# Kernel optimization log

Hardware: AMD Instinct MI355X
Metric: run time of the kernel (lower is better)

The kernel has to match this reference:

```python
import jax, jax.numpy as jnp
import numpy as np

HID = 768
POS = 768
TGT = 20
LBL = 30522
EPS = 1e-5


def layer_norm(x, g, b):
    mu = jnp.mean(x, axis=-1, keepdims=True)
    var = jnp.mean((x - mu) ** 2, axis=-1, keepdims=True)
    return (x - mu) * jax.lax.rsqrt(var + EPS) * g + b


def setup_inputs() -> dict:
    key = jax.random.key(0)
    ks = jax.random.split(key, 12)
    bs, n_node, num_pairs = 4, 512, 128
    inp = {
        "input_nodes": jax.random.normal(ks[0], (bs, n_node, HID), dtype=jnp.float32),
        "pairs": jax.random.randint(ks[1], (bs, num_pairs, 2), 0, n_node - 1, dtype=jnp.int64),
        "pos_emb": jax.random.normal(ks[2], (TGT, POS), dtype=jnp.float32) * 0.02,
        "W1": jax.random.normal(ks[3], (2 * HID + POS, HID), dtype=jnp.float32) * 0.02,
        "b1": jnp.zeros((HID,), dtype=jnp.float32),
        "g1": jnp.ones((HID,), dtype=jnp.float32),
        "be1": jnp.zeros((HID,), dtype=jnp.float32),
        "W2": jax.random.normal(ks[4], (HID, HID), dtype=jnp.float32) * 0.02,
        "b2": jnp.zeros((HID,), dtype=jnp.float32),
        "g2": jnp.ones((HID,), dtype=jnp.float32),
        "be2": jnp.zeros((HID,), dtype=jnp.float32),
        "Wd": jax.random.normal(ks[5], (HID, LBL), dtype=jnp.float32) * 0.02,
        "bd": jnp.zeros((LBL,), dtype=jnp.float32),
    }
    return inp


def reference(input_nodes, pairs, pos_emb, W1, b1, g1, be1, W2, b2, g2, be2, Wd, bd):
    bs, num_pairs, _ = pairs.shape
    dim = input_nodes.shape[-1]
    left = pairs[:, :, 0] + 1   # [bs, np]
    right = pairs[:, :, 1] + 1
    # gather paired node features: [bs, np, dim]
    lh = jnp.take_along_axis(input_nodes, left[:, :, None], axis=1)
    rh = jnp.take_along_axis(input_nodes, right[:, :, None], axis=1)
    R = bs * num_pairs
    lh = jnp.broadcast_to(lh.reshape(R, 1, dim), (R, TGT, dim))
    rh = jnp.broadcast_to(rh.reshape(R, 1, dim), (R, TGT, dim))
    pe = jnp.broadcast_to(pos_emb[None, :, :], (R, TGT, POS))
    x = jnp.concatenate((lh, rh, pe), axis=-1)  # [R, TGT, 2*HID+POS]
    h = layer_norm(jax.nn.gelu(x @ W1 + b1), g1, be1)
    h = layer_norm(jax.nn.gelu(h @ W2 + b2), g2, be2)
    return h @ Wd + bd  # [R, TGT, LBL]
```

## Files before the change

kernel.cpp:

```cpp
#include <hip/hip_runtime.h>
#include <stdint.h>
#include <math.h>

typedef unsigned short u16;
typedef unsigned int u32;

#define HID   768
#define TGT   20
#define LBL   30522
#define RPAIR 512
#define ROWS  10240
#define KCAT  1536
#define NPAD  30592

typedef float  f32x4  __attribute__((ext_vector_type(4)));
typedef __bf16 bf16x8 __attribute__((ext_vector_type(8)));

__device__ __forceinline__ u16 f2bf(float f) {
  u32 u = __float_as_uint(f);
  u += 0x7fffu + ((u >> 16) & 1u);
  return (u16)(u >> 16);
}
__device__ __forceinline__ float bf2f(u16 h) {
  return __uint_as_float(((u32)h) << 16);
}
__device__ __forceinline__ float gelu_tanh(float x) {
  float x3 = x * x * x;
  float t = tanhf(0.7978845608028654f * (x + 0.044715f * x3));
  return 0.5f * x * (1.0f + t);
}

__device__ __forceinline__ void async16(u16* lds, const u16* g) {
  __builtin_amdgcn_global_load_lds(
      (__attribute__((address_space(1))) void*)const_cast<u16*>(g),
      (__attribute__((address_space(3))) void*)lds,
      16, 0, 0);
}

#define BARRIER() do { asm volatile("" ::: "memory"); __builtin_amdgcn_s_barrier(); asm volatile("" ::: "memory"); } while (0)
#define VMW(N) do { asm volatile("s_waitcnt vmcnt(" #N ")" ::: "memory"); __builtin_amdgcn_sched_barrier(0); } while (0)

__global__ __launch_bounds__(256) void tconv_kernel(const float* __restrict__ B,
                                                    u16* __restrict__ Bt,
                                                    int K, int N, int Npad) {
  __shared__ u16 tile[32][34];
  int n0 = blockIdx.x * 32, k0 = blockIdx.y * 32;
  int tx = threadIdx.x & 31, ty = threadIdx.x >> 5;
#pragma unroll
  for (int i = 0; i < 4; i++) {
    int kk = ty + i * 8;
    int k = k0 + kk, n = n0 + tx;
    float v = (k < K && n < N) ? B[(size_t)k * N + n] : 0.0f;
    tile[kk][tx] = f2bf(v);
  }
  __syncthreads();
#pragma unroll
  for (int i = 0; i < 4; i++) {
    int nn = ty + i * 8;
    int n = n0 + nn, k = k0 + tx;
    if (n < Npad && k < K) Bt[(size_t)n * K + k] = tile[tx][nn];
  }
}

__global__ __launch_bounds__(256) void gather_kernel(const float* __restrict__ nodes,
                                                     const int* __restrict__ p32,
                                                     u16* __restrict__ A1) {
  int idx = blockIdx.x * 256 + threadIdx.x;
  if (idx >= RPAIR * KCAT) return;
  bool is64 = ((p32[1] | p32[3] | p32[5] | p32[7] | p32[9] | p32[11] | p32[13] | p32[15]) == 0);
  int r = idx / KCAT, c = idx - r * KCAT;
  int b = r >> 7, p = r & 127;
  int which = (c >= HID) ? 1 : 0;
  int cc = which ? (c - HID) : c;
  int slot = (b * 128 + p) * 2 + which;
  int node = (is64 ? p32[slot * 2] : p32[slot]) + 1;
  float v = nodes[((size_t)(b * 512 + node)) * HID + cc];
  A1[idx] = f2bf(v);
}

__global__ __launch_bounds__(256) void peproj_kernel(const float* __restrict__ pos_emb,
                                                     const float* __restrict__ W1,
                                                     const float* __restrict__ b1,
                                                     float* __restrict__ pep) {
  __shared__ float pe[HID];
  int t = blockIdx.x, tid = threadIdx.x;
  for (int i = tid; i < HID; i += 256) pe[i] = pos_emb[t * HID + i];
  __syncthreads();
  float acc0 = 0.f, acc1 = 0.f, acc2 = 0.f;
  const float* Wp = W1 + (size_t)KCAT * HID;
  for (int k = 0; k < HID; k++) {
    float p = pe[k];
    const float* wr = Wp + (size_t)k * HID;
    acc0 = fmaf(p, wr[tid], acc0);
    acc1 = fmaf(p, wr[tid + 256], acc1);
    acc2 = fmaf(p, wr[tid + 512], acc2);
  }
  pep[t * HID + tid]       = acc0 + b1[tid];
  pep[t * HID + tid + 256] = acc1 + b1[tid + 256];
  pep[t * HID + tid + 512] = acc2 + b1[tid + 512];
}

template <int EPI>
__global__ __launch_bounds__(256) void gemm_bt(const u16* __restrict__ A,
                                               const u16* __restrict__ Bt,
                                               const float* __restrict__ bias,
                                               float* __restrict__ Cf,
                                               u16* __restrict__ Cb,
                                               int N, int K) {
  __shared__ __align__(16) u16 As[128 * 32];
  __shared__ __align__(16) u16 Bs[128 * 32];
  const int tid  = threadIdx.x;
  const int lane = tid & 63;
  const int w    = tid >> 6;
  const int wr   = w >> 1, wc = w & 1;
  const int m0 = blockIdx.y * 128;
  const int n0 = blockIdx.x * 128;

  f32x4 acc[4][4];
  const f32x4 fzero = {0.f, 0.f, 0.f, 0.f};
#pragma unroll
  for (int m = 0; m < 4; m++)
#pragma unroll
    for (int n = 0; n < 4; n++) acc[m][n] = fzero;

  const int srow = lane >> 2;
  const int scol = (lane & 3) * 8;
  const int nkt = K >> 5;

  for (int kt = 0; kt < nkt; ++kt) {
    const int k0 = kt << 5;
#pragma unroll
    for (int j = 0; j < 2; j++) {
      int rbase = w * 32 + j * 16;
      async16(&As[rbase * 32], A + (size_t)(m0 + rbase + srow) * K + k0 + scol);
      async16(&Bs[rbase * 32], Bt + (size_t)(n0 + rbase + srow) * K + k0 + scol);
    }
    asm volatile("s_waitcnt vmcnt(0)" ::: "memory");
    __syncthreads();

    bf16x8 a[4], b[4];
    const int kk = (lane >> 4) * 8;
#pragma unroll
    for (int m = 0; m < 4; m++)
      a[m] = *reinterpret_cast<const bf16x8*>(&As[(wr * 64 + m * 16 + (lane & 15)) * 32 + kk]);
#pragma unroll
    for (int n = 0; n < 4; n++)
      b[n] = *reinterpret_cast<const bf16x8*>(&Bs[(wc * 64 + n * 16 + (lane & 15)) * 32 + kk]);
#pragma unroll
    for (int m = 0; m < 4; m++)
#pragma unroll
      for (int n = 0; n < 4; n++)
        acc[m][n] = __builtin_amdgcn_mfma_f32_16x16x32_bf16(a[m], b[n], acc[m][n], 0, 0, 0);
    __syncthreads();
  }

  const int rr = (lane >> 4) * 4;
  const int cc = lane & 15;
#pragma unroll
  for (int m = 0; m < 4; m++) {
#pragma unroll
    for (int n = 0; n < 4; n++) {
      int col = n0 + wc * 64 + n * 16 + cc;
#pragma unroll
      for (int j = 0; j < 4; j++) {
        int row = m0 + wr * 64 + m * 16 + rr + j;
        float v = acc[m][n][j];
        if (EPI == 0) {
          Cf[(size_t)row * N + col] = v;
        } else {
          v = gelu_tanh(v + bias[col]);
          Cb[(size_t)row * N + col] = f2bf(v);
        }
      }
    }
  }
}

__global__ __launch_bounds__(256) void gemm_head(const u16* __restrict__ A,
                                                 const u16* __restrict__ B,
                                                 const float* __restrict__ bias,
                                                 float* __restrict__ C) {
  __shared__ __align__(16) u16 As[2][128 * 32];
  __shared__ __align__(16) u16 Bs[2][128 * 32];
  const int tid  = threadIdx.x;
  const int lane = tid & 63;
  const int w    = tid >> 6;
  const int wr   = w >> 1, wc = w & 1;

  const int n0 = blockIdx.x * 128;
  const int m0 = blockIdx.y * 128;

  f32x4 acc[4][4];
  const f32x4 fzero = {0.f, 0.f, 0.f, 0.f};
#pragma unroll
  for (int m = 0; m < 4; m++)
#pragma unroll
    for (int n = 0; n < 4; n++) acc[m][n] = fzero;

  const int sr = lane >> 2;
  const int sc = ((lane & 3) ^ ((lane >> 3) & 3)) * 8;

  auto stage = [&](int buf, int kt) {
    const int k0 = kt << 5;
#pragma unroll
    for (int j = 0; j < 2; j++) {
      int rbase = w * 32 + j * 16;
      async16(&As[buf][rbase * 32], A + (size_t)(m0 + rbase + sr) * 768 + k0 + sc);
      async16(&Bs[buf][rbase * 32], B + (size_t)(n0 + rbase + sr) * 768 + k0 + sc);
    }
  };

  const int rr  = (lane >> 4) * 4;
  const int cc  = lane & 15;
  const int kch = lane >> 4;

  stage(0, 0);
  for (int t = 0; t < 24; ++t) {
    if (t < 23) { stage((t + 1) & 1, t + 1); VMW(4); }
    else        { VMW(0); }
    BARRIER();

    const u16* Ab = As[t & 1];
    const u16* Bb = Bs[t & 1];
    bf16x8 a[4], b[4];
#pragma unroll
    for (int m = 0; m < 4; m++) {
      int row = wr * 64 + m * 16 + cc;
      a[m] = *reinterpret_cast<const bf16x8*>(&Ab[row * 32 + ((kch ^ ((row >> 1) & 3)) << 3)]);
    }
#pragma unroll
    for (int n = 0; n < 4; n++) {
      int row = wc * 64 + n * 16 + cc;
      b[n] = *reinterpret_cast<const bf16x8*>(&Bb[row * 32 + ((kch ^ ((row >> 1) & 3)) << 3)]);
    }
#pragma unroll
    for (int m = 0; m < 4; m++)
#pragma unroll
      for (int n = 0; n < 4; n++)
        acc[m][n] = __builtin_amdgcn_mfma_f32_16x16x32_bf16(a[m], b[n], acc[m][n], 0, 0, 0);
    BARRIER();
  }

#pragma unroll
  for (int n = 0; n < 4; n++) {
    int col = n0 + wc * 64 + n * 16 + cc;
    if (col < LBL) {
      float bv = bias[col];
#pragma unroll
      for (int m = 0; m < 4; m++)
#pragma unroll
        for (int j = 0; j < 4; j++) {
          int row = m0 + wr * 64 + m * 16 + rr + j;
          C[(size_t)row * LBL + col] = acc[m][n][j] + bv;
        }
    }
  }
}

__global__ __launch_bounds__(256) void fuse1_kernel(const float* __restrict__ s,
                                                    const float* __restrict__ pep,
                                                    const float* __restrict__ g1,
                                                    const float* __restrict__ be1,
                                                    u16* __restrict__ h1) {
  __shared__ float red[8];
  int g = blockIdx.x, tid = threadIdx.x;
  int r = g / TGT, t = g - r * TGT;
  const float* sr = s + (size_t)r * HID;
  const float* pt = pep + (size_t)t * HID;
  float y[3], s1 = 0.f, s2 = 0.f;
#pragma unroll
  for (int i = 0; i < 3; i++) {
    int j = tid + i * 256;
    float x = sr[j] + pt[j];
    y[i] = gelu_tanh(x);
    s1 += y[i];
    s2 += y[i] * y[i];
  }
#pragma unroll
  for (int off = 32; off > 0; off >>= 1) {
    s1 += __shfl_down(s1, off);
    s2 += __shfl_down(s2, off);
  }
  if ((tid & 63) == 0) { red[tid >> 6] = s1; red[4 + (tid >> 6)] = s2; }
  __syncthreads();
  float mean = (red[0] + red[1] + red[2] + red[3]) * (1.0f / HID);
  float var  = (red[4] + red[5] + red[6] + red[7]) * (1.0f / HID) - mean * mean;
  float inv  = rsqrtf(var + 1e-5f);
#pragma unroll
  for (int i = 0; i < 3; i++) {
    int j = tid + i * 256;
    h1[(size_t)g * HID + j] = f2bf((y[i] - mean) * inv * g1[j] + be1[j]);
  }
}

__global__ __launch_bounds__(256) void fuse2_kernel(const u16* __restrict__ G,
                                                    const float* __restrict__ g2,
                                                    const float* __restrict__ be2,
                                                    u16* __restrict__ h2) {
  __shared__ float red[8];
  int g = blockIdx.x, tid = threadIdx.x;
  const u16* gr = G + (size_t)g * HID;
  float y[3], s1 = 0.f, s2 = 0.f;
#pragma unroll
  for (int i = 0; i < 3; i++) {
    int j = tid + i * 256;
    y[i] = bf2f(gr[j]);
    s1 += y[i];
    s2 += y[i] * y[i];
  }
#pragma unroll
  for (int off = 32; off > 0; off >>= 1) {
    s1 += __shfl_down(s1, off);
    s2 += __shfl_down(s2, off);
  }
  if ((tid & 63) == 0) { red[tid >> 6] = s1; red[4 + (tid >> 6)] = s2; }
  __syncthreads();
  float mean = (red[0] + red[1] + red[2] + red[3]) * (1.0f / HID);
  float var  = (red[4] + red[5] + red[6] + red[7]) * (1.0f / HID) - mean * mean;
  float inv  = rsqrtf(var + 1e-5f);
#pragma unroll
  for (int i = 0; i < 3; i++) {
    int j = tid + i * 256;
    h2[(size_t)g * HID + j] = f2bf((y[i] - mean) * inv * g2[j] + be2[j]);
  }
}

extern "C" void kernel_launch(void* const* d_in, const int* in_sizes, int n_in,
                              void* d_out, int out_size, void* d_ws, size_t ws_size,
                              hipStream_t stream) {
  const float* input_nodes = (const float*)d_in[0];
  const int*   pairs       = (const int*)d_in[1];
  const float* pos_emb     = (const float*)d_in[2];
  const float* W1  = (const float*)d_in[3];
  const float* b1  = (const float*)d_in[4];
  const float* g1  = (const float*)d_in[5];
  const float* be1 = (const float*)d_in[6];
  const float* W2  = (const float*)d_in[7];
  const float* b2  = (const float*)d_in[8];
  const float* g2  = (const float*)d_in[9];
  const float* be2 = (const float*)d_in[10];
  const float* Wd  = (const float*)d_in[11];
  const float* bd  = (const float*)d_in[12];
  float* out = (float*)d_out;

  char* ws = (char*)d_ws;
  u16*   WdT   = (u16*)(ws + 0);
  u16*   W2T   = (u16*)(ws + 46989312);
  u16*   W1lrT = (u16*)(ws + 48168960);
  u16*   A1    = (u16*)(ws + 50528256);
  float* pep   = (float*)(ws + 52101120);
  float* sbuf  = (float*)(ws + 52162560);
  u16*   h1    = (u16*)(ws + 53735424);
  u16*   G     = (u16*)(ws + 69464064);

  tconv_kernel<<<dim3(956, 24), 256, 0, stream>>>(Wd, WdT, HID, LBL, NPAD);
  tconv_kernel<<<dim3(24, 24), 256, 0, stream>>>(W2, W2T, HID, HID, HID);
  tconv_kernel<<<dim3(24, 48), 256, 0, stream>>>(W1, W1lrT, KCAT, HID, HID);
  gather_kernel<<<dim3((RPAIR * KCAT + 255) / 256), 256, 0, stream>>>(input_nodes, pairs, A1);
  peproj_kernel<<<dim3(TGT), 256, 0, stream>>>(pos_emb, W1, b1, pep);

  gemm_bt<0><<<dim3(6, 4), 256, 0, stream>>>(A1, W1lrT, nullptr, sbuf, nullptr, HID, KCAT);
  fuse1_kernel<<<dim3(ROWS), 256, 0, stream>>>(sbuf, pep, g1, be1, h1);

  gemm_bt<1><<<dim3(6, 80), 256, 0, stream>>>(h1, W2T, b2, nullptr, G, HID, HID);
  fuse2_kernel<<<dim3(ROWS), 256, 0, stream>>>(G, g2, be2, G);

  gemm_head<<<dim3(239, 80), 256, 0, stream>>>(G, WdT, bd, out);
}
```

Measured before the change: 1.090 ms.

## Enlarge head GEMM tiles to 256x256 with 16 waves and grouped block order

The vocabulary-projection GEMM now uses 256x256 output tiles computed by 1024-thread blocks (16 waves, each still owning 64x64). Blocks are launched on a 1D grid and remapped so that groups of 24 N-tiles sweep all M-tiles, which is meant to keep a slice of the transposed Wd resident in L2. The transposed Wd is padded to 30720 columns, and workspace offsets shift to fit. Larger tiles halve global reloads per FLOP but double LDS use and reduce the number of resident blocks, which may hurt latency hiding.

```diff
diff --git a/kernel.cpp b/kernel.cpp
--- a/kernel.cpp
+++ b/kernel.cpp
@@ -11,7 +11,7 @@
 #define RPAIR 512
 #define ROWS  10240
 #define KCAT  1536
-#define NPAD  30592
+#define NPAD2 30720
 
 typedef float  f32x4  __attribute__((ext_vector_type(4)));
 typedef __bf16 bf16x8 __attribute__((ext_vector_type(8)));
@@ -176,19 +176,25 @@
   }
 }
 
-__global__ __launch_bounds__(256) void gemm_head(const u16* __restrict__ A,
-                                                 const u16* __restrict__ B,
-                                                 const float* __restrict__ bias,
-                                                 float* __restrict__ C) {
-  __shared__ __align__(16) u16 As[2][128 * 32];
-  __shared__ __align__(16) u16 Bs[2][128 * 32];
+__global__ __launch_bounds__(1024) void gemm_head(const u16* __restrict__ A,
+                                                  const u16* __restrict__ B,
+                                                  const float* __restrict__ bias,
+                                                  float* __restrict__ C) {
+  __shared__ __align__(16) u16 As[2][256 * 32];
+  __shared__ __align__(16) u16 Bs[2][256 * 32];
   const int tid  = threadIdx.x;
   const int lane = tid & 63;
-  const int w    = tid >> 6;
-  const int wr   = w >> 1, wc = w & 1;
-
-  const int n0 = blockIdx.x * 128;
-  const int m0 = blockIdx.y * 128;
+  const int wid  = tid >> 6;
+  const int wm   = wid >> 2;
+  const int wn   = wid & 3;
+
+  const int bid   = blockIdx.x;
+  const int chunk = bid / 960;
+  const int u     = bid - chunk * 960;
+  const int mt    = u / 24;
+  const int nt    = chunk * 24 + (u - mt * 24);
+  const int m0 = mt * 256;
+  const int n0 = nt * 256;
 
   f32x4 acc[4][4];
   const f32x4 fzero = {0.f, 0.f, 0.f, 0.f};
@@ -202,12 +208,9 @@
 
   auto stage = [&](int buf, int kt) {
     const int k0 = kt << 5;
-#pragma unroll
-    for (int j = 0; j < 2; j++) {
-      int rbase = w * 32 + j * 16;
-      async16(&As[buf][rbase * 32], A + (size_t)(m0 + rbase + sr) * 768 + k0 + sc);
-      async16(&Bs[buf][rbase * 32], B + (size_t)(n0 + rbase + sr) * 768 + k0 + sc);
-    }
+    const int rbase = wid * 16;
+    async16(&As[buf][rbase * 32], A + (size_t)(m0 + rbase + sr) * 768 + k0 + sc);
+    async16(&Bs[buf][rbase * 32], B + (size_t)(n0 + rbase + sr) * 768 + k0 + sc);
   };
 
   const int rr  = (lane >> 4) * 4;
@@ -216,7 +219,7 @@
 
   stage(0, 0);
   for (int t = 0; t < 24; ++t) {
-    if (t < 23) { stage((t + 1) & 1, t + 1); VMW(4); }
+    if (t < 23) { stage((t + 1) & 1, t + 1); VMW(2); }
     else        { VMW(0); }
     BARRIER();
 
@@ -225,12 +228,12 @@
     bf16x8 a[4], b[4];
 #pragma unroll
     for (int m = 0; m < 4; m++) {
-      int row = wr * 64 + m * 16 + cc;
+      int row = wm * 64 + m * 16 + cc;
       a[m] = *reinterpret_cast<const bf16x8*>(&Ab[row * 32 + ((kch ^ ((row >> 1) & 3)) << 3)]);
     }
 #pragma unroll
     for (int n = 0; n < 4; n++) {
-      int row = wc * 64 + n * 16 + cc;
+      int row = wn * 64 + n * 16 + cc;
       b[n] = *reinterpret_cast<const bf16x8*>(&Bb[row * 32 + ((kch ^ ((row >> 1) & 3)) << 3)]);
     }
 #pragma unroll
@@ -243,14 +246,14 @@
 
 #pragma unroll
   for (int n = 0; n < 4; n++) {
-    int col = n0 + wc * 64 + n * 16 + cc;
+    int col = n0 + wn * 64 + n * 16 + cc;
     if (col < LBL) {
       float bv = bias[col];
 #pragma unroll
       for (int m = 0; m < 4; m++)
 #pragma unroll
         for (int j = 0; j < 4; j++) {
-          int row = m0 + wr * 64 + m * 16 + rr + j;
+          int row = m0 + wm * 64 + m * 16 + rr + j;
           C[(size_t)row * LBL + col] = acc[m][n][j] + bv;
         }
     }
@@ -345,15 +348,15 @@
 
   char* ws = (char*)d_ws;
   u16*   WdT   = (u16*)(ws + 0);
-  u16*   W2T   = (u16*)(ws + 46989312);
-  u16*   W1lrT = (u16*)(ws + 48168960);
-  u16*   A1    = (u16*)(ws + 50528256);
-  float* pep   = (float*)(ws + 52101120);
-  float* sbuf  = (float*)(ws + 52162560);
-  u16*   h1    = (u16*)(ws + 53735424);
-  u16*   G     = (u16*)(ws + 69464064);
-
-  tconv_kernel<<<dim3(956, 24), 256, 0, stream>>>(Wd, WdT, HID, LBL, NPAD);
+  u16*   W2T   = (u16*)(ws + 47185920);
+  u16*   W1lrT = (u16*)(ws + 48365568);
+  u16*   A1    = (u16*)(ws + 50724864);
+  float* pep   = (float*)(ws + 52297728);
+  float* sbuf  = (float*)(ws + 52359168);
+  u16*   h1    = (u16*)(ws + 53932032);
+  u16*   G     = (u16*)(ws + 69660672);
+
+  tconv_kernel<<<dim3(960, 24), 256, 0, stream>>>(Wd, WdT, HID, LBL, NPAD2);
   tconv_kernel<<<dim3(24, 24), 256, 0, stream>>>(W2, W2T, HID, HID, HID);
   tconv_kernel<<<dim3(24, 48), 256, 0, stream>>>(W1, W1lrT, KCAT, HID, HID);
   gather_kernel<<<dim3((RPAIR * KCAT + 255) / 256), 256, 0, stream>>>(input_nodes, pairs, A1);
@@ -365,5 +368,5 @@
   gemm_bt<1><<<dim3(6, 80), 256, 0, stream>>>(h1, W2T, b2, nullptr, G, HID, HID);
   fuse2_kernel<<<dim3(ROWS), 256, 0, stream>>>(G, g2, be2, G);
 
-  gemm_head<<<dim3(239, 80), 256, 0, stream>>>(G, WdT, bd, out);
-}
+  gemm_head<<<dim3(4800), 1024, 0, stream>>>(G, WdT, bd, out);
+}
```

New measurement: 1.172 ms. 7.5% more time.
